# Kernel optimization log

Measured on AMD Instinct MI355X. Metric: run time of the kernel, lower is better.

## Reference

```python
import jax, jax.numpy as jnp
import numpy as np

N_NODES = 131072       # 64 graphs * 2048 nodes
N_EDGES = 2097152      # avg degree 16
N_GRAPHS = 64
NODES_PER_GRAPH = 2048
D_IN = 128
D_EMB = 64
D_HID = 128
N_ACT = 2048


def setup_inputs() -> dict:
    key = jax.random.key(0)
    ks = jax.random.split(key, 12)
    s = lambda d: 1.0 / np.sqrt(d)
    return {
        "x": jax.random.normal(ks[0], (N_NODES, D_IN), dtype=jnp.float32),
        "edge_index": jax.random.randint(ks[1], (2, N_EDGES), 0, N_NODES, dtype=jnp.int32),
        "W1l": jax.random.normal(ks[2], (D_EMB, D_IN), dtype=jnp.float32) * s(D_IN),
        "b1l": jnp.zeros((D_EMB,), dtype=jnp.float32),
        "W1r": jax.random.normal(ks[3], (D_EMB, D_IN), dtype=jnp.float32) * s(D_IN),
        "W2l": jax.random.normal(ks[4], (D_EMB, D_EMB), dtype=jnp.float32) * s(D_EMB),
        "b2l": jnp.zeros((D_EMB,), dtype=jnp.float32),
        "W2r": jax.random.normal(ks[5], (D_EMB, D_EMB), dtype=jnp.float32) * s(D_EMB),
        "fc1_W": jax.random.normal(ks[6], (D_HID, D_EMB), dtype=jnp.float32) * s(D_EMB),
        "fc1_b": jnp.zeros((D_HID,), dtype=jnp.float32),
        "fc2_W": jax.random.normal(ks[7], (N_ACT, D_HID), dtype=jnp.float32) * s(D_HID),
        "fc2_b": jnp.zeros((N_ACT,), dtype=jnp.float32),
    }


def _sage_conv(x, src, dst, Wl, bl, Wr):
    # PyG SAGEConv (mean aggr): out = lin_l(mean_{j in N(i)} x_j) + lin_r(x_i)
    msg = x[src]                                              # [E, D] gather
    agg = jax.ops.segment_sum(msg, dst, num_segments=N_NODES)  # [N, D]
    cnt = jax.ops.segment_sum(jnp.ones((src.shape[0],), x.dtype), dst,
                              num_segments=N_NODES)
    mean = agg / jnp.maximum(cnt, 1.0)[:, None]
    return mean @ Wl.T + bl + x @ Wr.T


def reference(x, edge_index, W1l, b1l, W1r, W2l, b2l, W2r,
              fc1_W, fc1_b, fc2_W, fc2_b):
    src, dst = edge_index[0], edge_index[1]
    h1 = _sage_conv(x, src, dst, W1l, b1l, W1r)    # [N, D_EMB]
    h2 = _sage_conv(h1, src, dst, W2l, b2l, W2r)   # [N, D_EMB]
    g = h2.reshape(N_GRAPHS, NODES_PER_GRAPH, D_EMB).mean(axis=1)  # [B, D_EMB]
    h = jax.nn.relu(g @ fc1_W.T + fc1_b)
    q_values = h @ fc2_W.T + fc2_b                 # [B, N_ACT]
    return q_values
```

## Files before the change

kernel.cpp:

```cpp
#include <hip/hip_runtime.h>
#include <hip/hip_bf16.h>

#define D_IN 128
#define D_EMB 64

typedef float f32x2 __attribute__((ext_vector_type(2)));
typedef float f32x4v __attribute__((ext_vector_type(4)));
typedef short bf16x8 __attribute__((ext_vector_type(8)));

static __device__ __forceinline__ unsigned short f2bf(float f) {
  __hip_bfloat16 h = __float2bfloat16(f);
  return *(unsigned short*)&h;
}

__global__ __launch_bounds__(256) void wprep_mfma_k(const float* __restrict__ W,
                                                    unsigned short* __restrict__ out,
                                                    int K) {
  int tid = blockIdx.x * 256 + threadIdx.x;
  int total = (K / 32) * 4 * 64;
  if (tid >= total) return;
  int lane = tid & 63;
  int ct = (tid >> 6) & 3;
  int s = tid >> 8;
  int row = ct * 16 + (lane & 15);
  int kk = s * 32 + (lane >> 4) * 8;
  unsigned short tmp[8];
#pragma unroll
  for (int j = 0; j < 8; j++) tmp[j] = f2bf(W[row * K + kk + j]);
  *(uint4*)&out[(size_t)tid * 8] = *(uint4*)tmp;
}


__global__ __launch_bounds__(256) void bhist1_k(const int* __restrict__ key,
                                                int* __restrict__ bh, int E) {
  __shared__ int h[256];
  const int t = threadIdx.x;
  h[t] = 0;
  __syncthreads();
  const int base = blockIdx.x * 2048;
#pragma unroll
  for (int j = 0; j < 8; j++) {
    int e = base + j * 256 + t;
    if (e < E) atomicAdd(&h[key[e] >> 9], 1);
  }
  __syncthreads();
  bh[t * 1024 + blockIdx.x] = h[t];
}

__global__ __launch_bounds__(256) void scanA_k(int* __restrict__ bh,
                                               int* __restrict__ bintot) {
  __shared__ int sa[256], sb[256];
  const int t = threadIdx.x;
  int* row = bh + (size_t)blockIdx.x * 1024;
  int v0 = row[t * 4], v1 = row[t * 4 + 1], v2 = row[t * 4 + 2], v3 = row[t * 4 + 3];
  int sum = v0 + v1 + v2 + v3;
  sa[t] = sum;
  __syncthreads();
  int* in = sa;
  int* out = sb;
  for (int st = 1; st < 256; st <<= 1) {
    out[t] = in[t] + (t >= st ? in[t - st] : 0);
    __syncthreads();
    int* tmp = in; in = out; out = tmp;
  }
  int excl = in[t] - sum;
  row[t * 4] = excl;
  row[t * 4 + 1] = excl + v0;
  row[t * 4 + 2] = excl + v0 + v1;
  row[t * 4 + 3] = excl + v0 + v1 + v2;
  if (t == 255) bintot[blockIdx.x] = in[255];
}

__global__ __launch_bounds__(256) void scanB_k(const int* __restrict__ bintot,
                                               int* __restrict__ base) {
  __shared__ int sa[256], sb[256];
  const int t = threadIdx.x;
  int v = bintot[t];
  sa[t] = v;
  __syncthreads();
  int* in = sa;
  int* out = sb;
  for (int st = 1; st < 256; st <<= 1) {
    out[t] = in[t] + (t >= st ? in[t - st] : 0);
    __syncthreads();
    int* tmp = in; in = out; out = tmp;
  }
  base[t] = in[t] - v;
  if (t == 255) base[256] = in[255];
}

__global__ __launch_bounds__(256) void sfill_k(const int* __restrict__ src,
                                               const int* __restrict__ dst,
                                               const int* __restrict__ sh,
                                               const int* __restrict__ ssub,
                                               int* __restrict__ srcS,
                                               int* __restrict__ dstS, int E) {
  __shared__ int hA[256], hB[256], runCur[256], gb[256];
  __shared__ int scache[2048];
  __shared__ int dcache[2048];
  __shared__ int sortS[2048];
  __shared__ int sortD[2048];
  __shared__ unsigned short subb[2048];
  const int t = threadIdx.x;
  const int base = blockIdx.x * 2048;
  const int n = min(2048, E - base);
  hA[t] = 0;
  __syncthreads();
#pragma unroll
  for (int j = 0; j < 8; j++) {
    int idx = j * 256 + t;
    int e = base + idx;
    if (idx < n) {
      int s = src[e];
      scache[idx] = s;
      dcache[idx] = dst[e];
      atomicAdd(&hA[s >> 9], 1);
    }
  }
  __syncthreads();
  int cnt = hA[t];
  int* in = hA;
  int* out = hB;
  for (int st = 1; st < 256; st <<= 1) {
    out[t] = in[t] + (t >= st ? in[t - st] : 0);
    __syncthreads();
    int* tmp = in; in = out; out = tmp;
  }
  int rs = in[t] - cnt;
  __syncthreads();
  hB[t] = rs;
  runCur[t] = rs;
  gb[t] = ssub[t] + sh[t * 1024 + blockIdx.x];
  __syncthreads();
#pragma unroll
  for (int j = 0; j < 8; j++) {
    int idx = j * 256 + t;
    if (idx < n) {
      int s = scache[idx];
      int b = s >> 9;
      int lpos = atomicAdd(&runCur[b], 1);
      sortS[lpos] = s;
      sortD[lpos] = dcache[idx];
      subb[lpos] = (unsigned short)b;
    }
  }
  __syncthreads();
  for (int idx = t; idx < n; idx += 256) {
    int b = subb[idx];
    int g = gb[b] + idx - hB[b];
    srcS[g] = sortS[idx];
    dstS[g] = sortD[idx];
  }
}

__global__ __launch_bounds__(256) void bfill1_k(const int* __restrict__ src,
                                                const int* __restrict__ dst,
                                                const int* __restrict__ bh,
                                                const int* __restrict__ sbase,
                                                unsigned int* __restrict__ bkt,
                                                int E) {
  __shared__ int hA[256], hB[256], runCur[256], gb[256];
  __shared__ int dcache[2048];
  __shared__ unsigned int sorted[2048];
  __shared__ unsigned short subb[2048];
  const int t = threadIdx.x;
  const int base = blockIdx.x * 2048;
  const int n = min(2048, E - base);
  hA[t] = 0;
  __syncthreads();
#pragma unroll
  for (int j = 0; j < 8; j++) {
    int idx = j * 256 + t;
    int e = base + idx;
    if (idx < n) {
      int d = dst[e];
      dcache[idx] = d;
      atomicAdd(&hA[d >> 9], 1);
    }
  }
  __syncthreads();
  int cnt = hA[t];
  int* in = hA;
  int* out = hB;
  for (int st = 1; st < 256; st <<= 1) {
    out[t] = in[t] + (t >= st ? in[t - st] : 0);
    __syncthreads();
    int* tmp = in; in = out; out = tmp;
  }
  int rs = in[t] - cnt;
  __syncthreads();
  hB[t] = rs;
  runCur[t] = rs;
  gb[t] = sbase[t] + bh[t * 1024 + blockIdx.x];
  __syncthreads();
#pragma unroll
  for (int j = 0; j < 8; j++) {
    int idx = j * 256 + t;
    int e = base + idx;
    if (idx < n) {
      int d = dcache[idx];
      int b = d >> 9;
      int lpos = atomicAdd(&runCur[b], 1);
      sorted[lpos] = ((unsigned)(d & 511) << 17) | (unsigned)src[e];
      subb[lpos] = (unsigned short)b;
    }
  }
  __syncthreads();
  for (int idx = t; idx < n; idx += 256) {
    int b = subb[idx];
    bkt[gb[b] + idx - hB[b]] = sorted[idx];
  }
}

__global__ __launch_bounds__(256) void deg4_k(const unsigned int* __restrict__ bkt,
                                              const int* __restrict__ sbase,
                                              int* __restrict__ deg) {
  __shared__ int h[512];
  const int t = threadIdx.x;
  h[t] = 0;
  h[t + 256] = 0;
  __syncthreads();
  const int i = blockIdx.x;
  const int lo = sbase[i], hi = sbase[i + 1];
  for (int e = lo + t; e < hi; e += 256) atomicAdd(&h[bkt[e] >> 17], 1);
  __syncthreads();
  deg[i * 512 + t] = h[t];
  deg[i * 512 + t + 256] = h[t + 256];
}

__global__ __launch_bounds__(256) void blocksum_k(const int* __restrict__ deg,
                                                  int* __restrict__ bsum) {
  __shared__ int sm[256];
  int t = threadIdx.x;
  sm[t] = deg[blockIdx.x * 256 + t];
  __syncthreads();
  for (int s = 128; s > 0; s >>= 1) {
    if (t < s) sm[t] += sm[t + s];
    __syncthreads();
  }
  if (t == 0) bsum[blockIdx.x] = sm[0];
}

__global__ __launch_bounds__(256) void scanbsum_k(int* __restrict__ bsum) {
  __shared__ int a[512], b[512];
  int t = threadIdx.x;
  a[t] = bsum[t];
  a[t + 256] = bsum[t + 256];
  __syncthreads();
  int* in = a;
  int* out = b;
  for (int st = 1; st < 512; st <<= 1) {
    for (int i = t; i < 512; i += 256) out[i] = in[i] + (i >= st ? in[i - st] : 0);
    __syncthreads();
    int* tmp = in; in = out; out = tmp;
  }
  for (int i = t; i < 512; i += 256) bsum[i] = (i == 0) ? 0 : in[i - 1];
}

__global__ __launch_bounds__(256) void rowptr_k(const int* __restrict__ deg,
                                                const int* __restrict__ bsumEx,
                                                int* __restrict__ rowPtr,
                                                float* __restrict__ invdeg) {
  __shared__ int a[256], b[256];
  int t = threadIdx.x;
  int i = blockIdx.x * 256 + t;
  int d = deg[i];
  a[t] = d;
  __syncthreads();
  int* in = a;
  int* out = b;
  for (int st = 1; st < 256; st <<= 1) {
    out[t] = in[t] + (t >= st ? in[t - st] : 0);
    __syncthreads();
    int* tmp = in; in = out; out = tmp;
  }
  int incl = in[t] + bsumEx[blockIdx.x];
  rowPtr[i + 1] = incl;
  invdeg[i] = 1.0f / fmaxf((float)d, 1.0f);
  if (i == 0) rowPtr[0] = 0;
}

#define CSR_CAP 12032
__global__ __launch_bounds__(256) void scat4_k(const unsigned int* __restrict__ bkt,
                                               const int* __restrict__ sbase,
                                               const int* __restrict__ rowPtr,
                                               int* __restrict__ csr) {
  __shared__ int cur[512];
  __shared__ int cbuf[CSR_CAP];
  const int t = threadIdx.x;
  const int i = blockIdx.x;
  const int node0 = i * 512;
  const int base0 = rowPtr[node0];
  cur[t] = rowPtr[node0 + t] - base0;
  cur[t + 256] = rowPtr[node0 + t + 256] - base0;
  __syncthreads();
  const int lo = sbase[i], hi = sbase[i + 1];
  for (int e = lo + t; e < hi; e += 256) {
    unsigned v = bkt[e];
    int pos = atomicAdd(&cur[v >> 17], 1);
    int sval = (int)(v & 0x1FFFFu);
    if (pos < CSR_CAP) cbuf[pos] = sval;
    else csr[base0 + pos] = sval;
  }
  __syncthreads();
  const int cnt = rowPtr[node0 + 512] - base0;
  const int lim = cnt < CSR_CAP ? cnt : CSR_CAP;
  for (int idx = t; idx < lim; idx += 256) csr[base0 + idx] = cbuf[idx];
}

__global__ __launch_bounds__(256) void gemm1_k(const float4* __restrict__ x4,
                                               const unsigned short* __restrict__ wb1,
                                               const unsigned short* __restrict__ wb2,
                                               const float* __restrict__ bias2,
                                               unsigned char* __restrict__ out1,
                                               float* __restrict__ out2) {
  constexpr int K = 128, K4 = K / 4;
  const int t = threadIdx.x;
  const int lane = t & 63;
  const int wv = t >> 6;
  const int col = lane & 15;
  const int quad = lane >> 4;
  const int nb = blockIdx.x * 64;
  const int arow = nb + wv * 16 + col;
  f32x4v acc1[4], acc2[4];
#pragma unroll
  for (int ct = 0; ct < 4; ct++) {
    acc1[ct] = (f32x4v){0.f, 0.f, 0.f, 0.f};
    float bj = bias2[ct * 16 + col];
    acc2[ct] = (f32x4v){bj, bj, bj, bj};
  }
#pragma unroll
  for (int s = 0; s < K / 32; s++) {
    float4 f0 = x4[(size_t)arow * K4 + s * 8 + quad * 2];
    float4 f1 = x4[(size_t)arow * K4 + s * 8 + quad * 2 + 1];
    unsigned short h[8];
    h[0] = f2bf(f0.x); h[1] = f2bf(f0.y); h[2] = f2bf(f0.z); h[3] = f2bf(f0.w);
    h[4] = f2bf(f1.x); h[5] = f2bf(f1.y); h[6] = f2bf(f1.z); h[7] = f2bf(f1.w);
    bf16x8 a = *(const bf16x8*)h;
#pragma unroll
    for (int ct = 0; ct < 4; ct++) {
      bf16x8 b1 = *(const bf16x8*)&wb1[(size_t)((s * 4 + ct) * 64 + lane) * 8];
      acc1[ct] = __builtin_amdgcn_mfma_f32_16x16x32_bf16(a, b1, acc1[ct], 0, 0, 0);
      bf16x8 b2 = *(const bf16x8*)&wb2[(size_t)((s * 4 + ct) * 64 + lane) * 8];
      acc2[ct] = __builtin_amdgcn_mfma_f32_16x16x32_bf16(a, b2, acc2[ct], 0, 0, 0);
    }
  }
#pragma unroll
  for (int ct = 0; ct < 4; ct++) {
#pragma unroll
    for (int reg = 0; reg < 4; reg++) {
      int node = nb + wv * 16 + quad * 4 + reg;
      unsigned pk = (unsigned)__builtin_amdgcn_cvt_pk_fp8_f32(acc1[ct][reg],
                                                              acc1[ct][reg], 0, false);
      out1[(size_t)node * 64 + ct * 16 + col] = (unsigned char)(pk & 0xff);
      out2[(size_t)node * 64 + ct * 16 + col] = acc2[ct][reg];
    }
  }
}

#define LROW 72
template <int MODE>
__global__ __launch_bounds__(256) void gather_k(const uint4* __restrict__ yb,
                                                const int* __restrict__ csr,
                                                const int* __restrict__ rowPtr,
                                                const float* __restrict__ invdeg,
                                                const float4* __restrict__ xr,
                                                const unsigned short* __restrict__ wb2,
                                                unsigned char* __restrict__ y2,
                                                float* __restrict__ pm) {
  __shared__ float sg[4][4][16];
  __shared__ unsigned short sh1[64 * LROW];
  const int t = threadIdx.x;
  const int lane = t & 63;
  const int wv = t >> 6;
  const int q = lane & 3;
  const int nl = lane >> 2;
  const int nb = blockIdx.x * 64;
  const int n = nb + wv * 16 + nl;
  const int rp0 = rowPtr[n], rp1 = rowPtr[n + 1];
  float acc[16];
#pragma unroll
  for (int k = 0; k < 16; k++) acc[k] = 0.f;
  for (int e = rp0; e < rp1; e++) {
    int s = csr[e];
    uint4 v = yb[(size_t)s * 4 + q];
    f32x2 p;
    p = __builtin_amdgcn_cvt_pk_f32_fp8(v.x, false); acc[0] += p.x;  acc[1] += p.y;
    p = __builtin_amdgcn_cvt_pk_f32_fp8(v.x, true);  acc[2] += p.x;  acc[3] += p.y;
    p = __builtin_amdgcn_cvt_pk_f32_fp8(v.y, false); acc[4] += p.x;  acc[5] += p.y;
    p = __builtin_amdgcn_cvt_pk_f32_fp8(v.y, true);  acc[6] += p.x;  acc[7] += p.y;
    p = __builtin_amdgcn_cvt_pk_f32_fp8(v.z, false); acc[8] += p.x;  acc[9] += p.y;
    p = __builtin_amdgcn_cvt_pk_f32_fp8(v.z, true);  acc[10] += p.x; acc[11] += p.y;
    p = __builtin_amdgcn_cvt_pk_f32_fp8(v.w, false); acc[12] += p.x; acc[13] += p.y;
    p = __builtin_amdgcn_cvt_pk_f32_fp8(v.w, true);  acc[14] += p.x; acc[15] += p.y;
  }
  const float sc = invdeg[n];
  float gacc[16];
  if (MODE) {
    const int nloc = wv * 16 + nl;
    unsigned short hh[16];
#pragma unroll
    for (int u = 0; u < 4; u++) {
      float4 o = xr[(size_t)n * 16 + q * 4 + u];
      float v0 = acc[4 * u + 0] * sc + o.x;
      float v1 = acc[4 * u + 1] * sc + o.y;
      float v2 = acc[4 * u + 2] * sc + o.z;
      float v3 = acc[4 * u + 3] * sc + o.w;
      gacc[4 * u + 0] = v0; gacc[4 * u + 1] = v1;
      gacc[4 * u + 2] = v2; gacc[4 * u + 3] = v3;
      hh[4 * u + 0] = f2bf(v0); hh[4 * u + 1] = f2bf(v1);
      hh[4 * u + 2] = f2bf(v2); hh[4 * u + 3] = f2bf(v3);
    }
    *(uint4*)&sh1[nloc * LROW + q * 16] = *(uint4*)&hh[0];
    *(uint4*)&sh1[nloc * LROW + q * 16 + 8] = *(uint4*)&hh[8];
  } else {
#pragma unroll
    for (int k = 0; k < 16; k++) gacc[k] = acc[k] * sc;
  }
#pragma unroll
  for (int m = 4; m <= 32; m <<= 1)
#pragma unroll
    for (int k = 0; k < 16; k++) gacc[k] += __shfl_xor(gacc[k], m, 64);
  if (nl == 0) {
#pragma unroll
    for (int k = 0; k < 16; k++) sg[wv][q][k] = gacc[k];
  }
  __syncthreads();
  if (t < 64) {
    int qq = t >> 4, k = t & 15;
    float tot = sg[0][qq][k] + sg[1][qq][k] + sg[2][qq][k] + sg[3][qq][k];
    pm[((size_t)(blockIdx.x >> 5) * 32 + (blockIdx.x & 31)) * 64 + t] = tot;
  }
  if (MODE) {
    const int col = lane & 15;
    const int quad = lane >> 4;
    f32x4v a2[4];
#pragma unroll
    for (int ct = 0; ct < 4; ct++) a2[ct] = (f32x4v){0.f, 0.f, 0.f, 0.f};
#pragma unroll
    for (int s = 0; s < 2; s++) {
      bf16x8 a = *(const bf16x8*)&sh1[(wv * 16 + col) * LROW + s * 32 + quad * 8];
#pragma unroll
      for (int ct = 0; ct < 4; ct++) {
        bf16x8 b = *(const bf16x8*)&wb2[(size_t)((s * 4 + ct) * 64 + lane) * 8];
        a2[ct] = __builtin_amdgcn_mfma_f32_16x16x32_bf16(a, b, a2[ct], 0, 0, 0);
      }
    }
#pragma unroll
    for (int ct = 0; ct < 4; ct++) {
#pragma unroll
      for (int reg = 0; reg < 4; reg++) {
        int node = nb + wv * 16 + quad * 4 + reg;
        unsigned pk = (unsigned)__builtin_amdgcn_cvt_pk_fp8_f32(a2[ct][reg],
                                                                a2[ct][reg], 0, false);
        y2[(size_t)node * 64 + ct * 16 + col] = (unsigned char)(pk & 0xff);
      }
    }
  }
}

__global__ __launch_bounds__(256) void reduce_part_k(const float* __restrict__ pm,
                                                     float* __restrict__ gm) {
  int idx = blockIdx.x * 256 + threadIdx.x;
  int b = idx >> 6, j = idx & 63;
  float acc = 0.0f;
  for (int blk = 0; blk < 32; blk++) acc += pm[((size_t)b * 32 + blk) * 64 + j];
  gm[idx] = acc * (1.0f / 2048.0f);
}

__global__ __launch_bounds__(256) void combine_k(const float* __restrict__ gmean2,
                                                 const float* __restrict__ gmean1,
                                                 const float* __restrict__ b2l,
                                                 const float* __restrict__ W2r,
                                                 float* __restrict__ g) {
  int idx = blockIdx.x * 256 + threadIdx.x;
  int b = idx >> 6, j = idx & 63;
  const float4* m4 = (const float4*)(gmean1 + b * 64);
  const float4* w4 = (const float4*)(W2r + j * 64);
  float acc = gmean2[idx] + b2l[j];
#pragma unroll
  for (int k4 = 0; k4 < 16; k4++) {
    float4 mv = m4[k4], wv = w4[k4];
    acc += mv.x * wv.x + mv.y * wv.y + mv.z * wv.z + mv.w * wv.w;
  }
  g[idx] = acc;
}

__global__ __launch_bounds__(256) void mlp1_k(const float* __restrict__ g,
                                              const float* __restrict__ fc1_W,
                                              const float* __restrict__ fc1_b,
                                              float* __restrict__ h) {
  int idx = blockIdx.x * 256 + threadIdx.x;
  int b = idx >> 7, k = idx & 127;
  const float4* g4 = (const float4*)(g + b * 64);
  const float4* w4 = (const float4*)(fc1_W + k * 64);
  float acc = fc1_b[k];
#pragma unroll
  for (int j4 = 0; j4 < 16; j4++) {
    float4 gv = g4[j4], wv = w4[j4];
    acc += gv.x * wv.x + gv.y * wv.y + gv.z * wv.z + gv.w * wv.w;
  }
  h[idx] = fmaxf(acc, 0.0f);
}

__global__ __launch_bounds__(256) void mlp2_k(const float* __restrict__ h,
                                              const float* __restrict__ fc2_W,
                                              const float* __restrict__ fc2_b,
                                              float* __restrict__ out) {
  __shared__ float4 sh[32];
  int b = blockIdx.x >> 3;
  int a = (blockIdx.x & 7) * 256 + threadIdx.x;
  if (threadIdx.x < 32) sh[threadIdx.x] = ((const float4*)(h + b * 128))[threadIdx.x];
  __syncthreads();
  const float4* w4 = (const float4*)(fc2_W + (size_t)a * 128);
  float acc = fc2_b[a];
#pragma unroll
  for (int k4 = 0; k4 < 32; k4++) {
    float4 hv = sh[k4], wv = w4[k4];
    acc += hv.x * wv.x + hv.y * wv.y + hv.z * wv.z + hv.w * wv.w;
  }
  out[b * 2048 + a] = acc;
}

extern "C" void kernel_launch(void* const* d_in, const int* in_sizes, int n_in,
                              void* d_out, int out_size, void* d_ws, size_t ws_size,
                              hipStream_t stream) {
  const float* x     = (const float*)d_in[0];
  const int*   ei    = (const int*)d_in[1];
  const float* W1l   = (const float*)d_in[2];
  const float* b1l   = (const float*)d_in[3];
  const float* W1r   = (const float*)d_in[4];
  const float* W2l   = (const float*)d_in[5];
  const float* b2l   = (const float*)d_in[6];
  const float* W2r   = (const float*)d_in[7];
  const float* fc1_W = (const float*)d_in[8];
  const float* fc1_b = (const float*)d_in[9];
  const float* fc2_W = (const float*)d_in[10];
  const float* fc2_b = (const float*)d_in[11];
  float* out = (float*)d_out;

  const int N = in_sizes[0] / D_IN;
  const int E = in_sizes[1] / 2;
  const int* src = ei;
  const int* dst = ei + E;

  char* ws = (char*)d_ws;
  int*   deg    = (int*)ws;     ws += (size_t)N * 4;
  int*   rowPtr = (int*)ws;     ws += (size_t)(N + 256) * 4;
  int*   bsum   = (int*)ws;     ws += 512 * 4;
  float* invdeg = (float*)ws;   ws += (size_t)N * 4;
  float* gmean1 = (float*)ws;   ws += 4096 * 4;
  float* gmean2 = (float*)ws;   ws += 4096 * 4;
  float* g      = (float*)ws;   ws += 4096 * 4;
  float* hbuf   = (float*)ws;   ws += 8192 * 4;
  unsigned short* wb1l = (unsigned short*)ws;  ws += 8192 * 2;
  unsigned short* wb1r = (unsigned short*)ws;  ws += 8192 * 2;
  unsigned short* wb2l = (unsigned short*)ws;  ws += 4096 * 2;
  int*   sh     = (int*)ws;     ws += (size_t)256 * 1024 * 4;
  int*   bh     = (int*)ws;     ws += (size_t)256 * 1024 * 4;
  int*   tot    = (int*)ws;     ws += 256 * 4;
  int*   ssub   = (int*)ws;     ws += 260 * 4;
  int*   sbase  = (int*)ws;     ws += 260 * 4;
  float* p1     = (float*)ws;   ws += (size_t)64 * 32 * 64 * 4;
  float* p2     = (float*)ws;   ws += (size_t)64 * 32 * 64 * 4;
  unsigned int* bkt = (unsigned int*)ws;  ws += (size_t)E * 4;
  int*   csr    = (int*)ws;     ws += (size_t)E * 4;
  unsigned char* bufA = (unsigned char*)ws;  ws += (size_t)64 * N;
  unsigned char* bufD = (unsigned char*)ws;  ws += (size_t)64 * N;
  float* bufB   = (float*)ws;   ws += (size_t)64 * N * 4;
  size_t used = (size_t)(ws - (char*)d_ws);

  int* srcS = csr;
  int* dstS = (int*)bufA;

  hipMemsetAsync(d_ws, 0, used, stream);

  wprep_mfma_k<<<4, 256, 0, stream>>>(W1l, wb1l, 128);
  wprep_mfma_k<<<4, 256, 0, stream>>>(W1r, wb1r, 128);
  wprep_mfma_k<<<2, 256, 0, stream>>>(W2l, wb2l, 64);

  const int nch = (E + 2047) >> 11;
  bhist1_k<<<nch, 256, 0, stream>>>(src, sh, E);
  scanA_k<<<256, 256, 0, stream>>>(sh, tot);
  scanB_k<<<1, 256, 0, stream>>>(tot, ssub);
  sfill_k<<<nch, 256, 0, stream>>>(src, dst, sh, ssub, srcS, dstS, E);
  bhist1_k<<<nch, 256, 0, stream>>>(dstS, bh, E);
  scanA_k<<<256, 256, 0, stream>>>(bh, tot);
  scanB_k<<<1, 256, 0, stream>>>(tot, sbase);
  bfill1_k<<<nch, 256, 0, stream>>>(srcS, dstS, bh, sbase, bkt, E);
  deg4_k<<<256, 256, 0, stream>>>(bkt, sbase, deg);
  blocksum_k<<<N / 256, 256, 0, stream>>>(deg, bsum);
  scanbsum_k<<<1, 256, 0, stream>>>(bsum);
  rowptr_k<<<N / 256, 256, 0, stream>>>(deg, bsum, rowPtr, invdeg);
  scat4_k<<<256, 256, 0, stream>>>(bkt, sbase, rowPtr, csr);

  gemm1_k<<<N / 64, 256, 0, stream>>>((const float4*)x, wb1l, wb1r, b1l, bufA, bufB);
  gather_k<1><<<N / 64, 256, 0, stream>>>((const uint4*)bufA, csr, rowPtr, invdeg,
                                          (const float4*)bufB, wb2l, bufD, p1);
  reduce_part_k<<<16, 256, 0, stream>>>(p1, gmean1);

  gather_k<0><<<N / 64, 256, 0, stream>>>((const uint4*)bufD, csr, rowPtr, invdeg,
                                          nullptr, nullptr, nullptr, p2);
  reduce_part_k<<<16, 256, 0, stream>>>(p2, gmean2);

  combine_k<<<16, 256, 0, stream>>>(gmean2, gmean1, b2l, W2r, g);
  mlp1_k<<<32, 256, 0, stream>>>(g, fc1_W, fc1_b, hbuf);
  mlp2_k<<<512, 256, 0, stream>>>(hbuf, fc2_W, fc2_b, out);
}
```

Measured before the change: 356.3 us.

## Replace second-layer gather with src-ordered edge push into per-graph LDS sums

The second SAGE layer only feeds a per-graph mean, so its per-node neighbour gather is replaced by an edge-parallel push. Each edge carries a packed source id, destination graph and destination degree, and adds y[src]/deg[dst] into per-graph shared-memory accumulators. A final kernel reduces the 512 per-block partials. Because edges are walked in source-sorted order, reads of the second-layer features become nearly sequential instead of random. The trade-offs are an extra edge-packing pass, heavy LDS float atomics, a serial 512-way partial reduction, and a degree cap at 511 in the packed format.

```diff
diff --git a/kernel.cpp b/kernel.cpp
--- a/kernel.cpp
+++ b/kernel.cpp
@@ -308,6 +308,18 @@
   for (int idx = t; idx < lim; idx += 256) csr[base0 + idx] = cbuf[idx];
 }
 
+__global__ __launch_bounds__(256) void epb_k(const int* __restrict__ srcS,
+                                             const int* __restrict__ dstS,
+                                             const int* __restrict__ deg,
+                                             unsigned int* __restrict__ ep, int E) {
+  int e = blockIdx.x * 256 + threadIdx.x;
+  if (e >= E) return;
+  int s = srcS[e];
+  int d = dstS[e];
+  unsigned dg = (unsigned)min(deg[d], 511);
+  ep[e] = (unsigned)s | ((unsigned)(d >> 11) << 17) | (dg << 23);
+}
+
 __global__ __launch_bounds__(256) void gemm1_k(const float4* __restrict__ x4,
                                                const unsigned short* __restrict__ wb1,
                                                const unsigned short* __restrict__ wb2,
@@ -359,15 +371,14 @@
 }
 
 #define LROW 72
-template <int MODE>
-__global__ __launch_bounds__(256) void gather_k(const uint4* __restrict__ yb,
-                                                const int* __restrict__ csr,
-                                                const int* __restrict__ rowPtr,
-                                                const float* __restrict__ invdeg,
-                                                const float4* __restrict__ xr,
-                                                const unsigned short* __restrict__ wb2,
-                                                unsigned char* __restrict__ y2,
-                                                float* __restrict__ pm) {
+__global__ __launch_bounds__(256) void gatherf_k(const uint4* __restrict__ yb,
+                                                 const int* __restrict__ csr,
+                                                 const int* __restrict__ rowPtr,
+                                                 const float* __restrict__ invdeg,
+                                                 const float4* __restrict__ xr,
+                                                 const unsigned short* __restrict__ wb2,
+                                                 unsigned char* __restrict__ y2,
+                                                 float* __restrict__ pm) {
   __shared__ float sg[4][4][16];
   __shared__ unsigned short sh1[64 * LROW];
   const int t = threadIdx.x;
@@ -396,7 +407,7 @@
   }
   const float sc = invdeg[n];
   float gacc[16];
-  if (MODE) {
+  {
     const int nloc = wv * 16 + nl;
     unsigned short hh[16];
 #pragma unroll
@@ -413,9 +424,6 @@
     }
     *(uint4*)&sh1[nloc * LROW + q * 16] = *(uint4*)&hh[0];
     *(uint4*)&sh1[nloc * LROW + q * 16 + 8] = *(uint4*)&hh[8];
-  } else {
-#pragma unroll
-    for (int k = 0; k < 16; k++) gacc[k] = acc[k] * sc;
   }
 #pragma unroll
   for (int m = 4; m <= 32; m <<= 1)
@@ -431,7 +439,7 @@
     float tot = sg[0][qq][k] + sg[1][qq][k] + sg[2][qq][k] + sg[3][qq][k];
     pm[((size_t)(blockIdx.x >> 5) * 32 + (blockIdx.x & 31)) * 64 + t] = tot;
   }
-  if (MODE) {
+  {
     const int col = lane & 15;
     const int quad = lane >> 4;
     f32x4v a2[4];
@@ -457,6 +465,49 @@
       }
     }
   }
+}
+
+#define P2B 512
+__global__ __launch_bounds__(256) void push2_k(const uint4* __restrict__ yb,
+                                               const unsigned int* __restrict__ ep,
+                                               float* __restrict__ pp, int E) {
+  __shared__ float acc[64 * 65];
+  const int t = threadIdx.x;
+  for (int i = t; i < 64 * 65; i += 256) acc[i] = 0.f;
+  __syncthreads();
+  const int epb = (E + P2B - 1) / P2B;
+  const int lo = blockIdx.x * epb;
+  const int hi = min(E, lo + epb);
+  const int q = t & 3;
+  for (int e = lo + (t >> 2); e < hi; e += 64) {
+    unsigned v = ep[e];
+    int srcn = (int)(v & 0x1FFFFu);
+    int g = (int)((v >> 17) & 63u);
+    float w = 1.0f / fmaxf((float)(v >> 23), 1.0f);
+    uint4 y = yb[(size_t)srcn * 4 + q];
+    float* a = &acc[g * 65 + q * 16];
+    f32x2 p;
+    p = __builtin_amdgcn_cvt_pk_f32_fp8(y.x, false); atomicAdd(a + 0, p.x * w);  atomicAdd(a + 1, p.y * w);
+    p = __builtin_amdgcn_cvt_pk_f32_fp8(y.x, true);  atomicAdd(a + 2, p.x * w);  atomicAdd(a + 3, p.y * w);
+    p = __builtin_amdgcn_cvt_pk_f32_fp8(y.y, false); atomicAdd(a + 4, p.x * w);  atomicAdd(a + 5, p.y * w);
+    p = __builtin_amdgcn_cvt_pk_f32_fp8(y.y, true);  atomicAdd(a + 6, p.x * w);  atomicAdd(a + 7, p.y * w);
+    p = __builtin_amdgcn_cvt_pk_f32_fp8(y.z, false); atomicAdd(a + 8, p.x * w);  atomicAdd(a + 9, p.y * w);
+    p = __builtin_amdgcn_cvt_pk_f32_fp8(y.z, true);  atomicAdd(a + 10, p.x * w); atomicAdd(a + 11, p.y * w);
+    p = __builtin_amdgcn_cvt_pk_f32_fp8(y.w, false); atomicAdd(a + 12, p.x * w); atomicAdd(a + 13, p.y * w);
+    p = __builtin_amdgcn_cvt_pk_f32_fp8(y.w, true);  atomicAdd(a + 14, p.x * w); atomicAdd(a + 15, p.y * w);
+  }
+  __syncthreads();
+  for (int i = t; i < 4096; i += 256) {
+    pp[(size_t)blockIdx.x * 4096 + i] = acc[(i >> 6) * 65 + (i & 63)];
+  }
+}
+
+__global__ __launch_bounds__(256) void reduce2_k(const float* __restrict__ pp,
+                                                 float* __restrict__ gm) {
+  int idx = blockIdx.x * 256 + threadIdx.x;
+  float s = 0.0f;
+  for (int b = 0; b < P2B; b++) s += pp[(size_t)b * 4096 + idx];
+  gm[idx] = s * (1.0f / 2048.0f);
 }
 
 __global__ __launch_bounds__(256) void reduce_part_k(const float* __restrict__ pm,
@@ -562,7 +613,6 @@
   int*   ssub   = (int*)ws;     ws += 260 * 4;
   int*   sbase  = (int*)ws;     ws += 260 * 4;
   float* p1     = (float*)ws;   ws += (size_t)64 * 32 * 64 * 4;
-  float* p2     = (float*)ws;   ws += (size_t)64 * 32 * 64 * 4;
   unsigned int* bkt = (unsigned int*)ws;  ws += (size_t)E * 4;
   int*   csr    = (int*)ws;     ws += (size_t)E * 4;
   unsigned char* bufA = (unsigned char*)ws;  ws += (size_t)64 * N;
@@ -570,8 +620,10 @@
   float* bufB   = (float*)ws;   ws += (size_t)64 * N * 4;
   size_t used = (size_t)(ws - (char*)d_ws);
 
-  int* srcS = csr;
+  int* srcS = (int*)bufD;
   int* dstS = (int*)bufA;
+  unsigned int* ep = bkt;
+  float* pp = bufB;
 
   hipMemsetAsync(d_ws, 0, used, stream);
 
@@ -593,15 +645,15 @@
   scanbsum_k<<<1, 256, 0, stream>>>(bsum);
   rowptr_k<<<N / 256, 256, 0, stream>>>(deg, bsum, rowPtr, invdeg);
   scat4_k<<<256, 256, 0, stream>>>(bkt, sbase, rowPtr, csr);
+  epb_k<<<(E + 255) / 256, 256, 0, stream>>>(srcS, dstS, deg, ep, E);
 
   gemm1_k<<<N / 64, 256, 0, stream>>>((const float4*)x, wb1l, wb1r, b1l, bufA, bufB);
-  gather_k<1><<<N / 64, 256, 0, stream>>>((const uint4*)bufA, csr, rowPtr, invdeg,
-                                          (const float4*)bufB, wb2l, bufD, p1);
+  gatherf_k<<<N / 64, 256, 0, stream>>>((const uint4*)bufA, csr, rowPtr, invdeg,
+                                        (const float4*)bufB, wb2l, bufD, p1);
   reduce_part_k<<<16, 256, 0, stream>>>(p1, gmean1);
 
-  gather_k<0><<<N / 64, 256, 0, stream>>>((const uint4*)bufD, csr, rowPtr, invdeg,
-                                          nullptr, nullptr, nullptr, p2);
-  reduce_part_k<<<16, 256, 0, stream>>>(p2, gmean2);
+  push2_k<<<P2B, 256, 0, stream>>>((const uint4*)bufD, ep, pp, E);
+  reduce2_k<<<16, 256, 0, stream>>>(pp, gmean2);
 
   combine_k<<<16, 256, 0, stream>>>(gmean2, gmean1, b2l, W2r, g);
   mlp1_k<<<32, 256, 0, stream>>>(g, fc1_W, fc1_b, hbuf);
```

Result: slower. 1.015 ms (+184.8%).
